# Kernel optimization log

Hardware: AMD Instinct MI355X
Metric: run time of the kernel (lower is better)

## Reference

```python
import jax, jax.numpy as jnp
import numpy as np

B, S1, S2, D1, D2 = 4, 2048, 2048, 512, 512
H, DK, DV = 8, 64, 64


def setup_inputs() -> dict:
    key = jax.random.key(0)
    ks = jax.random.split(key, 8)
    x1 = jax.random.normal(ks[0], (B, S1, D1), dtype=jnp.float32)
    x2 = jax.random.normal(ks[1], (B, S2, D2), dtype=jnp.float32)
    x3 = jax.random.normal(ks[2], (B, S2, D2), dtype=jnp.float32)
    s = 0.02
    Wq = jax.random.normal(ks[3], (D1, H * DK), dtype=jnp.float32) * s
    Wk = jax.random.normal(ks[4], (D2, H * DK), dtype=jnp.float32) * s
    Wv = jax.random.normal(ks[5], (D2, H * DV), dtype=jnp.float32) * s
    Wo = jax.random.normal(ks[6], (H * DV, D1), dtype=jnp.float32) * s
    bo = jnp.zeros((D1,), dtype=jnp.float32)
    return {"x1": x1, "x2": x2, "x3": x3, "Wq": Wq, "Wk": Wk, "Wv": Wv, "Wo": Wo, "bo": bo}


def reference(x1, x2, x3, Wq, Wk, Wv, Wo, bo):
    b, s1, _ = x1.shape
    # project to per-head q, k, v: [B, H, S, Dh]
    q = (x1 @ Wq).reshape(b, s1, H, DK).transpose(0, 2, 1, 3)
    k = (x2 @ Wk).reshape(b, x2.shape[1], H, DK).transpose(0, 2, 1, 3)
    v = (x3 @ Wv).reshape(b, x3.shape[1], H, DV).transpose(0, 2, 1, 3)
    scores = jnp.einsum('bhqd,bhkd->bhqk', q, k) / jnp.sqrt(jnp.float32(DK))
    attn = jax.nn.softmax(scores, axis=-1)
    out = jnp.einsum('bhqk,bhkd->bhqd', attn, v)  # [B, H, S1, DV]
    out = out.transpose(0, 2, 1, 3).reshape(b, s1, H * DV)
    return out @ Wo + bo
```

## Files before the change

### kernel.cpp

```cpp
#include <hip/hip_runtime.h>

typedef __attribute__((ext_vector_type(4))) float f32x4;
typedef __attribute__((ext_vector_type(16))) float f32x16;
typedef __attribute__((ext_vector_type(8))) __bf16 bf16x8;
typedef __attribute__((ext_vector_type(4))) __bf16 bf16x4;
typedef __attribute__((ext_vector_type(2))) __bf16 bf16x2;
typedef __attribute__((ext_vector_type(4))) unsigned u32x4;

#define DEVINL __device__ __forceinline__

DEVINL void gld16(const void* g, void* l) {
  __builtin_amdgcn_global_load_lds((__attribute__((address_space(1))) void*)(void*)g,
                                   (__attribute__((address_space(3))) void*)l, 16, 0, 0);
}


__global__ __launch_bounds__(256) void cvt_w(const float* Wq, const float* Wk, const float* Wv,
                                             const float* Wo, __bf16* WT) {
  __shared__ float t[64][65];
  const int l = blockIdx.x;
  const int z = l >> 6;
  const float* W = z == 0 ? Wq : z == 1 ? Wk : z == 2 ? Wv : Wo;
  __bf16* D = WT + (size_t)z * 512 * 512;
  const int r0 = ((l >> 3) & 7) * 64, c0 = (l & 7) * 64;
  const int tx = threadIdx.x & 63, ty = threadIdx.x >> 6;
#pragma unroll
  for (int j = 0; j < 16; ++j)
    t[ty + j * 4][tx] = W[(size_t)(r0 + ty + j * 4) * 512 + c0 + tx];
  __syncthreads();
#pragma unroll
  for (int j = 0; j < 16; ++j)
    D[(size_t)(c0 + ty + j * 4) * 512 + r0 + tx] = (__bf16)t[tx][ty + j * 4];
}


DEVINL void gemm_tile_f32(const float* A, const __bf16* Bt, int m0, int n0,
                          __bf16* As, __bf16* Bs, f32x4 acc[4][4]) {
  const int tid = threadIdx.x, lane = tid & 63, w = tid >> 6;
  const int qd = lane >> 4, r = lane & 15;
  const int wm = w & 1, wn = w >> 1;
  const char* bp[4];
#pragma unroll
  for (int j = 0; j < 4; ++j) {
    int c = (w * 4 + j) * 64 + lane;
    int row = c >> 3, gc = (c & 7) ^ (row & 7);
    bp[j] = (const char*)Bt + (size_t)(n0 + row) * 1024 + gc * 16;
  }
  const int am = tid >> 4, ac = tid & 15;
  const float* ap = A + (size_t)(m0 + am) * 512 + ac * 4;
  int woff[8];
#pragma unroll
  for (int j = 0; j < 8; ++j) {
    int m = j * 16 + am;
    woff[j] = m * 128 + (((ac >> 1) ^ (m & 7)) << 4) + ((ac & 1) << 3);
  }
  int offA[4][2], offB[4][2];
#pragma unroll
  for (int t = 0; t < 4; ++t)
#pragma unroll
    for (int ks = 0; ks < 2; ++ks) {
      int m = wm * 64 + t * 16 + r;
      offA[t][ks] = m * 128 + (((ks * 4 + qd) ^ (m & 7)) * 16);
      int n = wn * 64 + t * 16 + r;
      offB[t][ks] = n * 128 + (((ks * 4 + qd) ^ (n & 7)) * 16);
    }
  char* AsC = (char*)As;
  char* BsC = (char*)Bs;
  f32x4 areg[8];
  auto loadA = [&](int kt) {
#pragma unroll
    for (int j = 0; j < 8; ++j)
      areg[j] = *(const f32x4*)(ap + (size_t)j * 16 * 512 + kt * 64);
  };
  loadA(0);
  for (int kt = 0; kt < 8; ++kt) {
    __syncthreads();
#pragma unroll
    for (int j = 0; j < 8; ++j) {
      bf16x4 o;
#pragma unroll
      for (int g = 0; g < 4; ++g) o[g] = (__bf16)areg[j][g];
      *(bf16x4*)(AsC + woff[j]) = o;
    }
#pragma unroll
    for (int j = 0; j < 4; ++j) gld16(bp[j] + kt * 128, BsC + (w * 4 + j) * 1024);
    if (kt < 7) loadA(kt + 1);
    __syncthreads();
#pragma unroll
    for (int ks = 0; ks < 2; ++ks) {
      bf16x8 a[4], b[4];
#pragma unroll
      for (int t = 0; t < 4; ++t) {
        a[t] = *(const bf16x8*)(AsC + offA[t][ks]);
        b[t] = *(const bf16x8*)(BsC + offB[t][ks]);
      }
#pragma unroll
      for (int i = 0; i < 4; ++i)
#pragma unroll
        for (int j2 = 0; j2 < 4; ++j2)
          acc[i][j2] = __builtin_amdgcn_mfma_f32_16x16x32_bf16(a[i], b[j2], acc[i][j2], 0, 0, 0);
    }
  }
}

__global__ __launch_bounds__(256, 3) void gemm_proj(const float* x1, const float* x2,
                                                    const float* x3, const __bf16* WT,
                                                    __bf16* Qo, __bf16* Ko, __bf16* Vto) {
  __shared__ __align__(16) char smem[34816];
  __bf16* As = (__bf16*)smem;
  __bf16* Bs = (__bf16*)(smem + 16384);
  const int z = blockIdx.z;
  const float* A = z == 0 ? x1 : z == 1 ? x2 : x3;
  const __bf16* Bt = WT + (size_t)z * 512 * 512;
  const int l = blockIdx.x;
  const int sidx = l >> 3;
  const int m0 = ((l & 7) * 8 + (sidx >> 2)) * 128;
  const int n0 = (sidx & 3) * 128;
  f32x4 acc[4][4] = {};
  gemm_tile_f32(A, Bt, m0, n0, As, Bs, acc);
  const int tid = threadIdx.x, lane = tid & 63, w = tid >> 6;
  const int qd = lane >> 4, r = lane & 15, wm = w & 1, wn = w >> 1;
  const int b = m0 >> 11, sbase = m0 & 2047;
  if (z == 2) {
    __syncthreads();
    char* T = smem;
#pragma unroll
    for (int mt = 0; mt < 4; ++mt)
#pragma unroll
      for (int nt = 0; nt < 4; ++nt) {
        int dv = wn * 64 + nt * 16 + r;
        int sl = wm * 64 + mt * 16 + qd * 4;
        bf16x4 p4;
#pragma unroll
        for (int g = 0; g < 4; ++g) p4[g] = (__bf16)acc[mt][nt][g];
        *(bf16x4*)(T + (size_t)dv * 272 + sl * 2) = p4;
      }
    __syncthreads();
#pragma unroll
    for (int p2 = 0; p2 < 2; ++p2) {
      int dvrow = p2 * 64 + (tid >> 2);
      int col = n0 + dvrow, h = col >> 6, d = col & 63;
      __bf16* dst = Vto + ((size_t)(b * 8 + h) * 64 + d) * 2048 + sbase + (tid & 3) * 8;
#pragma unroll
      for (int j = 0; j < 4; ++j) {
        bf16x8 vv = *(const bf16x8*)(T + (size_t)dvrow * 272 + (tid & 3) * 16 + j * 64);
        *(bf16x8*)(dst + j * 32) = vv;
      }
    }
  } else {
    const float qscale = 0.18033688f;
#pragma unroll
    for (int mt = 0; mt < 4; ++mt) {
#pragma unroll
      for (int nt = 0; nt < 4; ++nt) {
        f32x4 v = acc[mt][nt];
        if (z == 0) {
#pragma unroll
          for (int g = 0; g < 4; ++g) v[g] *= qscale;
        }
        int col = n0 + wn * 64 + nt * 16 + r;
        int h = col >> 6, d = col & 63;
        int s = sbase + wm * 64 + mt * 16 + qd * 4;
        __bf16* O = (z == 0 ? Qo : Ko) + ((size_t)(b * 8 + h) * 2048 + s) * 64 + d;
#pragma unroll
        for (int g = 0; g < 4; ++g) O[(size_t)g * 64] = (__bf16)v[g];
      }
    }
  }
}

__global__ __launch_bounds__(256, 2) void gemm_out(const __bf16* Op, const float* Lp,
                                                   const __bf16* WoT, const float* bo,
                                                   float* out) {
  __shared__ __align__(16) __bf16 As[64 * 64];
  __shared__ __align__(16) __bf16 Bs[128 * 64];
  const int tid = threadIdx.x, lane = tid & 63, w = tid >> 6;
  const int qd = lane >> 4, r = lane & 15, wm = w & 1, wn = w >> 1;
  const int id = blockIdx.x;
  const int rest = id >> 3;
  const int m0 = ((id & 7) * 16 + (rest & 15)) * 64;
  const int n0 = (rest >> 4) * 128;
  const int b8 = (m0 >> 11) * 8;
  const int sb = m0 & 2047;
  const char* bp[4];
#pragma unroll
  for (int j = 0; j < 4; ++j) {
    int c = (w * 4 + j) * 64 + lane;
    int row = c >> 3, gc = (c & 7) ^ (row & 7);
    bp[j] = (const char*)WoT + (size_t)(n0 + row) * 1024 + gc * 16;
  }
  int arow[2], ach[2];
#pragma unroll
  for (int j = 0; j < 2; ++j) {
    int c = (w * 2 + j) * 64 + lane;
    arow[j] = c >> 3;
    ach[j] = c & 7;
  }
  int offA[2][2], offB[4][2];
#pragma unroll
  for (int ks = 0; ks < 2; ++ks) {
#pragma unroll
    for (int t = 0; t < 2; ++t) {
      int m = wm * 32 + t * 16 + r;
      offA[t][ks] = m * 128 + (((ks * 4 + qd) ^ (m & 7)) * 16);
    }
#pragma unroll
    for (int t = 0; t < 4; ++t) {
      int n = wn * 64 + t * 16 + r;
      offB[t][ks] = n * 128 + (((ks * 4 + qd) ^ (n & 7)) * 16);
    }
  }
  char* AsC = (char*)As;
  char* BsC = (char*)Bs;
  bf16x8 pa0[2], pa1[2];
  float pinv[2];
  auto loadA = [&](int h) {
#pragma unroll
    for (int j = 0; j < 2; ++j) {
      size_t rr = (size_t)(b8 + h) * 2048 + sb + arow[j];
      const __bf16* p0 = Op + rr * 64 + ach[j] * 8;
      pa0[j] = *(const bf16x8*)p0;
      pa1[j] = *(const bf16x8*)(p0 + (size_t)32 * 2048 * 64);
      pinv[j] = 1.0f / (Lp[rr] + Lp[rr + 65536]);
    }
  };
  loadA(0);
  f32x4 acc[2][4] = {};
  for (int kt = 0; kt < 8; ++kt) {
    __syncthreads();
#pragma unroll
    for (int j = 0; j < 4; ++j) gld16(bp[j] + kt * 128, BsC + (w * 4 + j) * 1024);
#pragma unroll
    for (int j = 0; j < 2; ++j) {
      bf16x8 q;
#pragma unroll
      for (int k2 = 0; k2 < 8; ++k2)
        q[k2] = (__bf16)(((float)pa0[j][k2] + (float)pa1[j][k2]) * pinv[j]);
      *(bf16x8*)(AsC + arow[j] * 128 + (ach[j] ^ (arow[j] & 7)) * 16) = q;
    }
    __syncthreads();
    if (kt < 7) loadA(kt + 1);
#pragma unroll
    for (int ks = 0; ks < 2; ++ks) {
      bf16x8 a[2], b[4];
#pragma unroll
      for (int t = 0; t < 2; ++t) a[t] = *(const bf16x8*)(AsC + offA[t][ks]);
#pragma unroll
      for (int t = 0; t < 4; ++t) b[t] = *(const bf16x8*)(BsC + offB[t][ks]);
#pragma unroll
      for (int i = 0; i < 2; ++i)
#pragma unroll
        for (int j2 = 0; j2 < 4; ++j2)
          acc[i][j2] = __builtin_amdgcn_mfma_f32_16x16x32_bf16(a[i], b[j2], acc[i][j2], 0, 0, 0);
    }
  }
#pragma unroll
  for (int nt = 0; nt < 4; ++nt) {
    int col = n0 + wn * 64 + nt * 16 + r;
    float bv = bo[col];
#pragma unroll
    for (int mt = 0; mt < 2; ++mt) {
      int mg = m0 + wm * 32 + mt * 16 + qd * 4;
#pragma unroll
      for (int g = 0; g < 4; ++g) out[(size_t)(mg + g) * 512 + col] = acc[mt][nt][g] + bv;
    }
  }
}

__global__ __launch_bounds__(256, 4) void attn(const __bf16* Q, const __bf16* K,
                                               const __bf16* Vt, __bf16* Opart, float* Lp) {
  __shared__ __align__(16) __bf16 Qs[128 * 64];
  __shared__ __align__(16) __bf16 Ksd[2][64 * 64];
  __shared__ __align__(16) __bf16 Vs[64 * 64];
  const int tid = threadIdx.x, lane = tid & 63, w = tid >> 6;
  const int l31 = lane & 31, lh = lane >> 5;
  const int id = blockIdx.x;
  const int rest = id >> 3;
  const int bh = (id & 7) * 4 + (rest >> 5);
  const int kvh = (rest >> 4) & 1;
  const int q0 = (rest & 15) * 128;
  const char* QgC = (const char*)(Q + ((size_t)bh * 2048 + q0) * 64);
  const char* KgC = (const char*)(K + (size_t)bh * 2048 * 64);
  const char* VgC = (const char*)(Vt + (size_t)bh * 64 * 2048);
  char* QsC = (char*)Qs;
  char* VsC = (char*)Vs;
  char* Kc = (char*)Ksd;
  char* Kn = (char*)Ksd + 8192;

  int koff[2], voff[2], ldso[2];
#pragma unroll
  for (int j = 0; j < 2; ++j) {
    int c = (w * 2 + j) * 64 + lane;
    int m = c >> 3, gc = (c & 7) ^ (m & 7);
    int ms = (m & ~12) | ((m & 4) << 1) | ((m & 8) >> 1);
    koff[j] = ms * 128 + gc * 16;
    voff[j] = m * 4096 + gc * 16;
    ldso[j] = (w * 2 + j) * 1024;
  }

  const int kt0 = kvh * 16;
  const size_t kb = (size_t)kt0 * 8192;
  const size_t vb = (size_t)kt0 * 128;

#pragma unroll
  for (int j = 0; j < 4; ++j) {
    int c = (w * 4 + j) * 64 + lane;
    int m = c >> 3, gc = (c & 7) ^ (m & 7);
    gld16(QgC + m * 128 + gc * 16, QsC + (w * 4 + j) * 1024);
  }
  gld16(KgC + kb + koff[0], Kc + ldso[0]);
  gld16(KgC + kb + koff[1], Kc + ldso[1]);
  gld16(VgC + vb + voff[0], VsC + ldso[0]);
  gld16(VgC + vb + voff[1], VsC + ldso[1]);
  gld16(KgC + kb + 8192 + koff[0], Kn + ldso[0]);
  gld16(KgC + kb + 8192 + koff[1], Kn + ldso[1]);
  __builtin_amdgcn_sched_barrier(0);
  asm volatile("s_waitcnt vmcnt(2)" ::: "memory");
  __builtin_amdgcn_sched_barrier(0);
  __builtin_amdgcn_s_barrier();
  __builtin_amdgcn_sched_barrier(0);

  const int rb = l31 * 128;
  const int he = (((lane & 7) ^ lh) << 4);
  const int qrow = (w * 32 + l31) * 128;

  bf16x8 ones;
#pragma unroll
  for (int j = 0; j < 8; ++j) ones[j] = (__bf16)1.0f;

  f32x16 oacc[2] = {};
  f32x16 lacc = {};
  bf16x8 pa[4];

  auto smhalf = [&](const f32x16& s, bf16x8& pa0, bf16x8& pa1) {
    unsigned wds[8];
#pragma unroll
    for (int i = 0; i < 8; ++i) {
      bf16x2 t;
      t[0] = (__bf16)__builtin_exp2f(s[2 * i]);
      t[1] = (__bf16)__builtin_exp2f(s[2 * i + 1]);
      wds[i] = __builtin_bit_cast(unsigned, t);
    }
    pa0 = __builtin_bit_cast(bf16x8, (u32x4){wds[0], wds[1], wds[2], wds[3]});
    pa1 = __builtin_bit_cast(bf16x8, (u32x4){wds[4], wds[5], wds[6], wds[7]});
  };
  auto qkchain = [&](const char* Kb, int half, const bf16x8 qf[4]) {
    f32x16 s = {};
#pragma unroll
    for (int c = 0; c < 4; ++c) {
      bf16x8 kf = *(const bf16x8*)(Kb + half * 4096 + rb + ((c << 5) ^ he));
      s = __builtin_amdgcn_mfma_f32_32x32x16_bf16(kf, qf[c], s, 0, 0, 0);
    }
    return s;
  };

  {
    bf16x8 qf[4];
#pragma unroll
    for (int c = 0; c < 4; ++c) qf[c] = *(const bf16x8*)(QsC + qrow + ((c << 5) ^ he));
    f32x16 s0 = qkchain(Kc, 0, qf);
    f32x16 s1 = qkchain(Kc, 1, qf);
    smhalf(s0, pa[0], pa[1]);
    smhalf(s1, pa[2], pa[3]);
  }
  __builtin_amdgcn_sched_barrier(0);
  asm volatile("s_waitcnt vmcnt(0)" ::: "memory");
  __builtin_amdgcn_sched_barrier(0);
  __builtin_amdgcn_s_barrier();
  __builtin_amdgcn_sched_barrier(0);

#pragma unroll 1
  for (int t = 0; t < 15; ++t) {
    __builtin_amdgcn_s_setprio(1);
#pragma unroll
    for (int c = 0; c < 4; ++c) {
      lacc = __builtin_amdgcn_mfma_f32_32x32x16_bf16(pa[c], ones, lacc, 0, 0, 0);
      bf16x8 vf0 = *(const bf16x8*)(VsC + rb + ((c << 5) ^ he));
      oacc[0] = __builtin_amdgcn_mfma_f32_32x32x16_bf16(pa[c], vf0, oacc[0], 0, 0, 0);
      bf16x8 vf1 = *(const bf16x8*)(VsC + 4096 + rb + ((c << 5) ^ he));
      oacc[1] = __builtin_amdgcn_mfma_f32_32x32x16_bf16(pa[c], vf1, oacc[1], 0, 0, 0);
    }
    bf16x8 qf[4];
#pragma unroll
    for (int c = 0; c < 4; ++c) qf[c] = *(const bf16x8*)(QsC + qrow + ((c << 5) ^ he));
    f32x16 s0 = qkchain(Kn, 0, qf);
    f32x16 s1 = qkchain(Kn, 1, qf);
    smhalf(s0, pa[0], pa[1]);
    __builtin_amdgcn_s_setprio(0);
    __builtin_amdgcn_sched_barrier(0);
    __builtin_amdgcn_s_barrier();
    __builtin_amdgcn_sched_barrier(0);

    gld16(VgC + vb + (size_t)(t + 1) * 128 + voff[0], VsC + ldso[0]);
    gld16(VgC + vb + (size_t)(t + 1) * 128 + voff[1], VsC + ldso[1]);
    if (t < 14) {
      gld16(KgC + kb + (size_t)(t + 2) * 8192 + koff[0], Kc + ldso[0]);
      gld16(KgC + kb + (size_t)(t + 2) * 8192 + koff[1], Kc + ldso[1]);
    }
    __builtin_amdgcn_sched_barrier(0);
    smhalf(s1, pa[2], pa[3]);
    __builtin_amdgcn_sched_barrier(0);
    asm volatile("s_waitcnt vmcnt(0)" ::: "memory");
    __builtin_amdgcn_sched_barrier(0);
    __builtin_amdgcn_s_barrier();
    __builtin_amdgcn_sched_barrier(0);

    char* tmp = Kc;
    Kc = Kn;
    Kn = tmp;
  }

#pragma unroll
  for (int c = 0; c < 4; ++c) {
    lacc = __builtin_amdgcn_mfma_f32_32x32x16_bf16(pa[c], ones, lacc, 0, 0, 0);
    bf16x8 vf0 = *(const bf16x8*)(VsC + rb + ((c << 5) ^ he));
    oacc[0] = __builtin_amdgcn_mfma_f32_32x32x16_bf16(pa[c], vf0, oacc[0], 0, 0, 0);
    bf16x8 vf1 = *(const bf16x8*)(VsC + 4096 + rb + ((c << 5) ^ he));
    oacc[1] = __builtin_amdgcn_mfma_f32_32x32x16_bf16(pa[c], vf1, oacc[1], 0, 0, 0);
  }

  const size_t pbase = (size_t)(kvh * 32 + bh) * 2048;
  if (l31 == 0) {
#pragma unroll
    for (int g = 0; g < 16; ++g)
      Lp[pbase + q0 + w * 32 + (g & 3) + 8 * (g >> 2) + 4 * lh] = lacc[g];
  }
  __bf16* Ob0 = Opart + pbase * 64;
#pragma unroll
  for (int dvt = 0; dvt < 2; ++dvt) {
#pragma unroll
    for (int g = 0; g < 16; ++g) {
      int s = q0 + w * 32 + (g & 3) + 8 * (g >> 2) + 4 * lh;
      Ob0[(size_t)s * 64 + dvt * 32 + l31] = (__bf16)oacc[dvt][g];
    }
  }
}


extern "C" void kernel_launch(void* const* d_in, const int* in_sizes, int n_in,
                              void* d_out, int out_size, void* d_ws, size_t ws_size,
                              hipStream_t stream) {
  const float* x1 = (const float*)d_in[0];
  const float* x2 = (const float*)d_in[1];
  const float* x3 = (const float*)d_in[2];
  const float* Wq = (const float*)d_in[3];
  const float* Wk = (const float*)d_in[4];
  const float* Wv = (const float*)d_in[5];
  const float* Wo = (const float*)d_in[6];
  const float* bo = (const float*)d_in[7];
  float* out = (float*)d_out;
  char* ws = (char*)d_ws;
  const size_t MB = 1ull << 20;
  __bf16* WT = (__bf16*)(ws + 24 * MB);
  __bf16* Qb = (__bf16*)(ws + 26 * MB);
  __bf16* Kb = (__bf16*)(ws + 34 * MB);
  __bf16* Vtb = (__bf16*)(ws + 42 * MB);
  __bf16* Opart = (__bf16*)(ws + 58 * MB);
  float* Lp = (float*)(ws + 74 * MB);

  cvt_w<<<dim3(256), 256, 0, stream>>>(Wq, Wk, Wv, Wo, WT);
  gemm_proj<<<dim3(256, 1, 3), 256, 0, stream>>>(x1, x2, x3, WT, Qb, Kb, Vtb);
  attn<<<dim3(1024), 256, 0, stream>>>(Qb, Kb, Vtb, Opart, Lp);
  gemm_out<<<dim3(512), 256, 0, stream>>>(Opart, Lp, WT + 3ull * 512 * 512, bo, out);
}
```

Measured before the change: 184.7 us.

## Enlarge attention blocks to 512 threads with 128-key tiles and register-held Q

The attention kernel now runs 512 blocks of 8 waves, each covering 256 query rows and 128-key K/V tiles, so every K/V tile staged in shared memory is shared by twice as many waves. Q fragments are loaded straight from global memory into registers once, which removes the Q shared-memory buffer, and the loop runs 7 iterations instead of 15, halving the barriers per key. The cost is more shared memory per block (48KB) and more registers (8 P fragments), which may lower occupancy under the 512-thread launch bound.

```diff
diff --git a/kernel.cpp b/kernel.cpp
--- a/kernel.cpp
+++ b/kernel.cpp
@@ -267,62 +267,61 @@
   }
 }
 
-__global__ __launch_bounds__(256, 4) void attn(const __bf16* Q, const __bf16* K,
+__global__ __launch_bounds__(512, 4) void attn(const __bf16* Q, const __bf16* K,
                                                const __bf16* Vt, __bf16* Opart, float* Lp) {
-  __shared__ __align__(16) __bf16 Qs[128 * 64];
-  __shared__ __align__(16) __bf16 Ksd[2][64 * 64];
-  __shared__ __align__(16) __bf16 Vs[64 * 64];
+  __shared__ __align__(16) __bf16 Ksd[2][128 * 64];
+  __shared__ __align__(16) __bf16 Vs[128 * 64];
   const int tid = threadIdx.x, lane = tid & 63, w = tid >> 6;
   const int l31 = lane & 31, lh = lane >> 5;
   const int id = blockIdx.x;
   const int rest = id >> 3;
-  const int bh = (id & 7) * 4 + (rest >> 5);
-  const int kvh = (rest >> 4) & 1;
-  const int q0 = (rest & 15) * 128;
-  const char* QgC = (const char*)(Q + ((size_t)bh * 2048 + q0) * 64);
-  const char* KgC = (const char*)(K + (size_t)bh * 2048 * 64);
-  const char* VgC = (const char*)(Vt + (size_t)bh * 64 * 2048);
-  char* QsC = (char*)Qs;
+  const int bh = (id & 7) * 4 + (rest >> 4);
+  const int kvh = (rest >> 3) & 1;
+  const int q0 = (rest & 7) * 256;
+  const char* QgC = (const char*)Q + ((size_t)bh * 2048 + q0) * 128;
+  const char* KgC = (const char*)K + (size_t)bh * 2048 * 128;
+  const char* VgC = (const char*)Vt + (size_t)bh * 64 * 4096;
   char* VsC = (char*)Vs;
   char* Kc = (char*)Ksd;
-  char* Kn = (char*)Ksd + 8192;
-
-  int koff[2], voff[2], ldso[2];
+  char* Kn = (char*)Ksd + 16384;
+
+  int ldso[2];
+  const char* kst[2];
+  const char* vst[2];
 #pragma unroll
   for (int j = 0; j < 2; ++j) {
-    int c = (w * 2 + j) * 64 + lane;
-    int m = c >> 3, gc = (c & 7) ^ (m & 7);
+    int o = ((w * 2 + j) * 64 + lane) * 16;
+    int tk = o >> 13;
+    int oo = o & 8191;
+    int m = oo >> 7;
+    int cs = (oo >> 4) & 7;
+    int gc = cs ^ (m & 7);
     int ms = (m & ~12) | ((m & 4) << 1) | ((m & 8) >> 1);
-    koff[j] = ms * 128 + gc * 16;
-    voff[j] = m * 4096 + gc * 16;
-    ldso[j] = (w * 2 + j) * 1024;
-  }
-
-  const int kt0 = kvh * 16;
-  const size_t kb = (size_t)kt0 * 8192;
-  const size_t vb = (size_t)kt0 * 128;
-
-#pragma unroll
-  for (int j = 0; j < 4; ++j) {
-    int c = (w * 4 + j) * 64 + lane;
-    int m = c >> 3, gc = (c & 7) ^ (m & 7);
-    gld16(QgC + m * 128 + gc * 16, QsC + (w * 4 + j) * 1024);
-  }
-  gld16(KgC + kb + koff[0], Kc + ldso[0]);
-  gld16(KgC + kb + koff[1], Kc + ldso[1]);
-  gld16(VgC + vb + voff[0], VsC + ldso[0]);
-  gld16(VgC + vb + voff[1], VsC + ldso[1]);
-  gld16(KgC + kb + 8192 + koff[0], Kn + ldso[0]);
-  gld16(KgC + kb + 8192 + koff[1], Kn + ldso[1]);
-  __builtin_amdgcn_sched_barrier(0);
-  asm volatile("s_waitcnt vmcnt(2)" ::: "memory");
+    kst[j] = KgC + (size_t)kvh * 16 * 8192 + (size_t)tk * 8192 + ms * 128 + gc * 16;
+    vst[j] = VgC + (size_t)m * 4096 + (size_t)kvh * 16 * 128 + tk * 128 + gc * 16;
+    ldso[j] = o;
+  }
+
+  const int qrow = (w * 32 + l31) * 128;
+  bf16x8 qf[4];
+#pragma unroll
+  for (int c = 0; c < 4; ++c)
+    qf[c] = *(const bf16x8*)(QgC + qrow + c * 32 + lh * 16);
+
+  gld16(kst[0], Kc + ldso[0]);
+  gld16(kst[1], Kc + ldso[1]);
+  gld16(vst[0], VsC + ldso[0]);
+  gld16(vst[1], VsC + ldso[1]);
+  gld16(kst[0] + 16384, Kn + ldso[0]);
+  gld16(kst[1] + 16384, Kn + ldso[1]);
+  __builtin_amdgcn_sched_barrier(0);
+  asm volatile("s_waitcnt vmcnt(4)" ::: "memory");
   __builtin_amdgcn_sched_barrier(0);
   __builtin_amdgcn_s_barrier();
   __builtin_amdgcn_sched_barrier(0);
 
   const int rb = l31 * 128;
   const int he = (((lane & 7) ^ lh) << 4);
-  const int qrow = (w * 32 + l31) * 128;
 
   bf16x8 ones;
 #pragma unroll
@@ -330,9 +329,9 @@
 
   f32x16 oacc[2] = {};
   f32x16 lacc = {};
-  bf16x8 pa[4];
-
-  auto smhalf = [&](const f32x16& s, bf16x8& pa0, bf16x8& pa1) {
+  bf16x8 pa[8];
+
+  auto smtile = [&](const f32x16& s, bf16x8& a0, bf16x8& a1) {
     unsigned wds[8];
 #pragma unroll
     for (int i = 0; i < 8; ++i) {
@@ -341,27 +340,28 @@
       t[1] = (__bf16)__builtin_exp2f(s[2 * i + 1]);
       wds[i] = __builtin_bit_cast(unsigned, t);
     }
-    pa0 = __builtin_bit_cast(bf16x8, (u32x4){wds[0], wds[1], wds[2], wds[3]});
-    pa1 = __builtin_bit_cast(bf16x8, (u32x4){wds[4], wds[5], wds[6], wds[7]});
+    a0 = __builtin_bit_cast(bf16x8, (u32x4){wds[0], wds[1], wds[2], wds[3]});
+    a1 = __builtin_bit_cast(bf16x8, (u32x4){wds[4], wds[5], wds[6], wds[7]});
   };
-  auto qkchain = [&](const char* Kb, int half, const bf16x8 qf[4]) {
+  auto qktile = [&](const char* base) {
     f32x16 s = {};
 #pragma unroll
     for (int c = 0; c < 4; ++c) {
-      bf16x8 kf = *(const bf16x8*)(Kb + half * 4096 + rb + ((c << 5) ^ he));
+      bf16x8 kf = *(const bf16x8*)(base + rb + ((c << 5) ^ he));
       s = __builtin_amdgcn_mfma_f32_32x32x16_bf16(kf, qf[c], s, 0, 0, 0);
     }
     return s;
   };
 
   {
-    bf16x8 qf[4];
-#pragma unroll
-    for (int c = 0; c < 4; ++c) qf[c] = *(const bf16x8*)(QsC + qrow + ((c << 5) ^ he));
-    f32x16 s0 = qkchain(Kc, 0, qf);
-    f32x16 s1 = qkchain(Kc, 1, qf);
-    smhalf(s0, pa[0], pa[1]);
-    smhalf(s1, pa[2], pa[3]);
+    f32x16 s0 = qktile(Kc);
+    smtile(s0, pa[0], pa[1]);
+    f32x16 s1 = qktile(Kc + 4096);
+    smtile(s1, pa[2], pa[3]);
+    f32x16 s2 = qktile(Kc + 8192);
+    smtile(s2, pa[4], pa[5]);
+    f32x16 s3 = qktile(Kc + 12288);
+    smtile(s3, pa[6], pa[7]);
   }
   __builtin_amdgcn_sched_barrier(0);
   asm volatile("s_waitcnt vmcnt(0)" ::: "memory");
@@ -370,35 +370,39 @@
   __builtin_amdgcn_sched_barrier(0);
 
 #pragma unroll 1
-  for (int t = 0; t < 15; ++t) {
+  for (int p = 0; p < 7; ++p) {
     __builtin_amdgcn_s_setprio(1);
 #pragma unroll
-    for (int c = 0; c < 4; ++c) {
-      lacc = __builtin_amdgcn_mfma_f32_32x32x16_bf16(pa[c], ones, lacc, 0, 0, 0);
-      bf16x8 vf0 = *(const bf16x8*)(VsC + rb + ((c << 5) ^ he));
-      oacc[0] = __builtin_amdgcn_mfma_f32_32x32x16_bf16(pa[c], vf0, oacc[0], 0, 0, 0);
-      bf16x8 vf1 = *(const bf16x8*)(VsC + 4096 + rb + ((c << 5) ^ he));
-      oacc[1] = __builtin_amdgcn_mfma_f32_32x32x16_bf16(pa[c], vf1, oacc[1], 0, 0, 0);
-    }
-    bf16x8 qf[4];
-#pragma unroll
-    for (int c = 0; c < 4; ++c) qf[c] = *(const bf16x8*)(QsC + qrow + ((c << 5) ^ he));
-    f32x16 s0 = qkchain(Kn, 0, qf);
-    f32x16 s1 = qkchain(Kn, 1, qf);
-    smhalf(s0, pa[0], pa[1]);
+    for (int st = 0; st < 2; ++st)
+#pragma unroll
+      for (int c = 0; c < 4; ++c) {
+        const int i = st * 4 + c;
+        lacc = __builtin_amdgcn_mfma_f32_32x32x16_bf16(pa[i], ones, lacc, 0, 0, 0);
+        bf16x8 vf0 = *(const bf16x8*)(VsC + st * 8192 + rb + ((c << 5) ^ he));
+        oacc[0] = __builtin_amdgcn_mfma_f32_32x32x16_bf16(pa[i], vf0, oacc[0], 0, 0, 0);
+        bf16x8 vf1 = *(const bf16x8*)(VsC + st * 8192 + 4096 + rb + ((c << 5) ^ he));
+        oacc[1] = __builtin_amdgcn_mfma_f32_32x32x16_bf16(pa[i], vf1, oacc[1], 0, 0, 0);
+      }
+    f32x16 s0 = qktile(Kn);
+    smtile(s0, pa[0], pa[1]);
+    f32x16 s1 = qktile(Kn + 4096);
+    smtile(s1, pa[2], pa[3]);
+    f32x16 s2 = qktile(Kn + 8192);
+    smtile(s2, pa[4], pa[5]);
+    f32x16 s3 = qktile(Kn + 12288);
     __builtin_amdgcn_s_setprio(0);
     __builtin_amdgcn_sched_barrier(0);
     __builtin_amdgcn_s_barrier();
     __builtin_amdgcn_sched_barrier(0);
 
-    gld16(VgC + vb + (size_t)(t + 1) * 128 + voff[0], VsC + ldso[0]);
-    gld16(VgC + vb + (size_t)(t + 1) * 128 + voff[1], VsC + ldso[1]);
-    if (t < 14) {
-      gld16(KgC + kb + (size_t)(t + 2) * 8192 + koff[0], Kc + ldso[0]);
-      gld16(KgC + kb + (size_t)(t + 2) * 8192 + koff[1], Kc + ldso[1]);
-    }
-    __builtin_amdgcn_sched_barrier(0);
-    smhalf(s1, pa[2], pa[3]);
+    gld16(vst[0] + (size_t)(p + 1) * 256, VsC + ldso[0]);
+    gld16(vst[1] + (size_t)(p + 1) * 256, VsC + ldso[1]);
+    if (p < 6) {
+      gld16(kst[0] + (size_t)(p + 2) * 16384, Kc + ldso[0]);
+      gld16(kst[1] + (size_t)(p + 2) * 16384, Kc + ldso[1]);
+    }
+    __builtin_amdgcn_sched_barrier(0);
+    smtile(s3, pa[6], pa[7]);
     __builtin_amdgcn_sched_barrier(0);
     asm volatile("s_waitcnt vmcnt(0)" ::: "memory");
     __builtin_amdgcn_sched_barrier(0);
@@ -411,13 +415,16 @@
   }
 
 #pragma unroll
-  for (int c = 0; c < 4; ++c) {
-    lacc = __builtin_amdgcn_mfma_f32_32x32x16_bf16(pa[c], ones, lacc, 0, 0, 0);
-    bf16x8 vf0 = *(const bf16x8*)(VsC + rb + ((c << 5) ^ he));
-    oacc[0] = __builtin_amdgcn_mfma_f32_32x32x16_bf16(pa[c], vf0, oacc[0], 0, 0, 0);
-    bf16x8 vf1 = *(const bf16x8*)(VsC + 4096 + rb + ((c << 5) ^ he));
-    oacc[1] = __builtin_amdgcn_mfma_f32_32x32x16_bf16(pa[c], vf1, oacc[1], 0, 0, 0);
-  }
+  for (int st = 0; st < 2; ++st)
+#pragma unroll
+    for (int c = 0; c < 4; ++c) {
+      const int i = st * 4 + c;
+      lacc = __builtin_amdgcn_mfma_f32_32x32x16_bf16(pa[i], ones, lacc, 0, 0, 0);
+      bf16x8 vf0 = *(const bf16x8*)(VsC + st * 8192 + rb + ((c << 5) ^ he));
+      oacc[0] = __builtin_amdgcn_mfma_f32_32x32x16_bf16(pa[i], vf0, oacc[0], 0, 0, 0);
+      bf16x8 vf1 = *(const bf16x8*)(VsC + st * 8192 + 4096 + rb + ((c << 5) ^ he));
+      oacc[1] = __builtin_amdgcn_mfma_f32_32x32x16_bf16(pa[i], vf1, oacc[1], 0, 0, 0);
+    }
 
   const size_t pbase = (size_t)(kvh * 32 + bh) * 2048;
   if (l31 == 0) {
@@ -460,6 +467,6 @@
 
   cvt_w<<<dim3(256), 256, 0, stream>>>(Wq, Wk, Wv, Wo, WT);
   gemm_proj<<<dim3(256, 1, 3), 256, 0, stream>>>(x1, x2, x3, WT, Qb, Kb, Vtb);
-  attn<<<dim3(1024), 256, 0, stream>>>(Qb, Kb, Vtb, Opart, Lp);
+  attn<<<dim3(512), 512, 0, stream>>>(Qb, Kb, Vtb, Opart, Lp);
   gemm_out<<<dim3(512), 256, 0, stream>>>(Opart, Lp, WT + 3ull * 512 * 512, bo, out);
 }
```

Result: slower. 235.6 us (+27.6%).

## Load V fragments directly from global memory instead of staging through LDS

Applied to the files above, without the earlier changes.

Removes the V shared-memory tile and its async global-to-LDS copies; each lane now reads its V fragments straight from global memory (Vt layout) inside the PV MFMA loop. Q fragments are hoisted out of the loop into registers, and the loop is restructured so the mid-iteration barrier disappears, leaving one barrier per tile. This cuts LDS footprint and synchronisation, but adds global-load latency directly on the MFMA critical path and more register pressure.

```diff
diff --git a/kernel.cpp b/kernel.cpp
--- a/kernel.cpp
+++ b/kernel.cpp
@@ -271,7 +271,6 @@
                                                const __bf16* Vt, __bf16* Opart, float* Lp) {
   __shared__ __align__(16) __bf16 Qs[128 * 64];
   __shared__ __align__(16) __bf16 Ksd[2][64 * 64];
-  __shared__ __align__(16) __bf16 Vs[64 * 64];
   const int tid = threadIdx.x, lane = tid & 63, w = tid >> 6;
   const int l31 = lane & 31, lh = lane >> 5;
   const int id = blockIdx.x;
@@ -283,24 +282,21 @@
   const char* KgC = (const char*)(K + (size_t)bh * 2048 * 64);
   const char* VgC = (const char*)(Vt + (size_t)bh * 64 * 2048);
   char* QsC = (char*)Qs;
-  char* VsC = (char*)Vs;
   char* Kc = (char*)Ksd;
   char* Kn = (char*)Ksd + 8192;
 
-  int koff[2], voff[2], ldso[2];
+  int koff[2], ldso[2];
 #pragma unroll
   for (int j = 0; j < 2; ++j) {
     int c = (w * 2 + j) * 64 + lane;
     int m = c >> 3, gc = (c & 7) ^ (m & 7);
     int ms = (m & ~12) | ((m & 4) << 1) | ((m & 8) >> 1);
     koff[j] = ms * 128 + gc * 16;
-    voff[j] = m * 4096 + gc * 16;
     ldso[j] = (w * 2 + j) * 1024;
   }
 
   const int kt0 = kvh * 16;
   const size_t kb = (size_t)kt0 * 8192;
-  const size_t vb = (size_t)kt0 * 128;
 
 #pragma unroll
   for (int j = 0; j < 4; ++j) {
@@ -310,8 +306,6 @@
   }
   gld16(KgC + kb + koff[0], Kc + ldso[0]);
   gld16(KgC + kb + koff[1], Kc + ldso[1]);
-  gld16(VgC + vb + voff[0], VsC + ldso[0]);
-  gld16(VgC + vb + voff[1], VsC + ldso[1]);
   gld16(KgC + kb + 8192 + koff[0], Kn + ldso[0]);
   gld16(KgC + kb + 8192 + koff[1], Kn + ldso[1]);
   __builtin_amdgcn_sched_barrier(0);
@@ -324,6 +318,13 @@
   const int he = (((lane & 7) ^ lh) << 4);
   const int qrow = (w * 32 + l31) * 128;
 
+  bf16x8 qf[4];
+#pragma unroll
+  for (int c = 0; c < 4; ++c) qf[c] = *(const bf16x8*)(QsC + qrow + ((c << 5) ^ he));
+
+  const char* vp0 = VgC + (size_t)l31 * 4096 + lh * 16 + (size_t)kt0 * 128;
+  const char* vp1 = vp0 + (size_t)32 * 4096;
+
   bf16x8 ones;
 #pragma unroll
   for (int j = 0; j < 8; ++j) ones[j] = (__bf16)1.0f;
@@ -332,7 +333,7 @@
   f32x16 lacc = {};
   bf16x8 pa[4];
 
-  auto smhalf = [&](const f32x16& s, bf16x8& pa0, bf16x8& pa1) {
+  auto smhalf = [&](const f32x16& s, bf16x8& a0, bf16x8& a1) {
     unsigned wds[8];
 #pragma unroll
     for (int i = 0; i < 8; ++i) {
@@ -341,10 +342,10 @@
       t[1] = (__bf16)__builtin_exp2f(s[2 * i + 1]);
       wds[i] = __builtin_bit_cast(unsigned, t);
     }
-    pa0 = __builtin_bit_cast(bf16x8, (u32x4){wds[0], wds[1], wds[2], wds[3]});
-    pa1 = __builtin_bit_cast(bf16x8, (u32x4){wds[4], wds[5], wds[6], wds[7]});
+    a0 = __builtin_bit_cast(bf16x8, (u32x4){wds[0], wds[1], wds[2], wds[3]});
+    a1 = __builtin_bit_cast(bf16x8, (u32x4){wds[4], wds[5], wds[6], wds[7]});
   };
-  auto qkchain = [&](const char* Kb, int half, const bf16x8 qf[4]) {
+  auto qkchain = [&](const char* Kb, int half) {
     f32x16 s = {};
 #pragma unroll
     for (int c = 0; c < 4; ++c) {
@@ -355,11 +356,8 @@
   };
 
   {
-    bf16x8 qf[4];
-#pragma unroll
-    for (int c = 0; c < 4; ++c) qf[c] = *(const bf16x8*)(QsC + qrow + ((c << 5) ^ he));
-    f32x16 s0 = qkchain(Kc, 0, qf);
-    f32x16 s1 = qkchain(Kc, 1, qf);
+    f32x16 s0 = qkchain(Kc, 0);
+    f32x16 s1 = qkchain(Kc, 1);
     smhalf(s0, pa[0], pa[1]);
     smhalf(s1, pa[2], pa[3]);
   }
@@ -371,34 +369,27 @@
 
 #pragma unroll 1
   for (int t = 0; t < 15; ++t) {
-    __builtin_amdgcn_s_setprio(1);
-#pragma unroll
-    for (int c = 0; c < 4; ++c) {
-      lacc = __builtin_amdgcn_mfma_f32_32x32x16_bf16(pa[c], ones, lacc, 0, 0, 0);
-      bf16x8 vf0 = *(const bf16x8*)(VsC + rb + ((c << 5) ^ he));
-      oacc[0] = __builtin_amdgcn_mfma_f32_32x32x16_bf16(pa[c], vf0, oacc[0], 0, 0, 0);
-      bf16x8 vf1 = *(const bf16x8*)(VsC + 4096 + rb + ((c << 5) ^ he));
-      oacc[1] = __builtin_amdgcn_mfma_f32_32x32x16_bf16(pa[c], vf1, oacc[1], 0, 0, 0);
-    }
-    bf16x8 qf[4];
-#pragma unroll
-    for (int c = 0; c < 4; ++c) qf[c] = *(const bf16x8*)(QsC + qrow + ((c << 5) ^ he));
-    f32x16 s0 = qkchain(Kn, 0, qf);
-    f32x16 s1 = qkchain(Kn, 1, qf);
-    smhalf(s0, pa[0], pa[1]);
-    __builtin_amdgcn_s_setprio(0);
-    __builtin_amdgcn_sched_barrier(0);
-    __builtin_amdgcn_s_barrier();
-    __builtin_amdgcn_sched_barrier(0);
-
-    gld16(VgC + vb + (size_t)(t + 1) * 128 + voff[0], VsC + ldso[0]);
-    gld16(VgC + vb + (size_t)(t + 1) * 128 + voff[1], VsC + ldso[1]);
     if (t < 14) {
       gld16(KgC + kb + (size_t)(t + 2) * 8192 + koff[0], Kc + ldso[0]);
       gld16(KgC + kb + (size_t)(t + 2) * 8192 + koff[1], Kc + ldso[1]);
     }
     __builtin_amdgcn_sched_barrier(0);
+
+    __builtin_amdgcn_s_setprio(1);
+#pragma unroll
+    for (int c = 0; c < 4; ++c) {
+      lacc = __builtin_amdgcn_mfma_f32_32x32x16_bf16(pa[c], ones, lacc, 0, 0, 0);
+      bf16x8 vf0 = *(const bf16x8*)(vp0 + c * 32);
+      oacc[0] = __builtin_amdgcn_mfma_f32_32x32x16_bf16(pa[c], vf0, oacc[0], 0, 0, 0);
+      bf16x8 vf1 = *(const bf16x8*)(vp1 + c * 32);
+      oacc[1] = __builtin_amdgcn_mfma_f32_32x32x16_bf16(pa[c], vf1, oacc[1], 0, 0, 0);
+    }
+    f32x16 s0 = qkchain(Kn, 0);
+    f32x16 s1 = qkchain(Kn, 1);
+    smhalf(s0, pa[0], pa[1]);
+    __builtin_amdgcn_s_setprio(0);
     smhalf(s1, pa[2], pa[3]);
+
     __builtin_amdgcn_sched_barrier(0);
     asm volatile("s_waitcnt vmcnt(0)" ::: "memory");
     __builtin_amdgcn_sched_barrier(0);
@@ -408,14 +399,16 @@
     char* tmp = Kc;
     Kc = Kn;
     Kn = tmp;
+    vp0 += 128;
+    vp1 += 128;
   }
 
 #pragma unroll
   for (int c = 0; c < 4; ++c) {
     lacc = __builtin_amdgcn_mfma_f32_32x32x16_bf16(pa[c], ones, lacc, 0, 0, 0);
-    bf16x8 vf0 = *(const bf16x8*)(VsC + rb + ((c << 5) ^ he));
+    bf16x8 vf0 = *(const bf16x8*)(vp0 + c * 32);
     oacc[0] = __builtin_amdgcn_mfma_f32_32x32x16_bf16(pa[c], vf0, oacc[0], 0, 0, 0);
-    bf16x8 vf1 = *(const bf16x8*)(VsC + 4096 + rb + ((c << 5) ^ he));
+    bf16x8 vf1 = *(const bf16x8*)(vp1 + c * 32);
     oacc[1] = __builtin_amdgcn_mfma_f32_32x32x16_bf16(pa[c], vf1, oacc[1], 0, 0, 0);
   }
 
```

New measurement: 208.0 us. +12.6%, slower.
